# Kernel optimization log

Measured on AMD Instinct MI355X. Metric: run time of the kernel, lower is better.

## Reference

```python
import jax, jax.numpy as jnp
import numpy as np

N_NODES = 50000
N_EDGES = 800000
IN_DIM = 128
HIDDEN = 128
OUT_DIM = 40


def setup_inputs() -> dict:
    key = jax.random.key(0)
    ks = jax.random.split(key, 6)
    x = jax.random.normal(ks[0], (N_NODES, IN_DIM), dtype=jnp.float32)
    edge_src = jax.random.randint(ks[1], (N_EDGES,), 0, N_NODES, dtype=jnp.int32)
    edge_dst = jax.random.randint(ks[2], (N_EDGES,), 0, N_NODES, dtype=jnp.int32)
    edge_weight = jax.random.uniform(ks[3], (N_EDGES,), dtype=jnp.float32)
    W1 = jax.random.normal(ks[4], (IN_DIM, HIDDEN), dtype=jnp.float32) / np.sqrt(IN_DIM)
    b1 = jnp.zeros((HIDDEN,), dtype=jnp.float32)
    W2 = jax.random.normal(ks[5], (HIDDEN, OUT_DIM), dtype=jnp.float32) / np.sqrt(HIDDEN)
    b2 = jnp.zeros((OUT_DIM,), dtype=jnp.float32)
    return {"x": x, "edge_src": edge_src, "edge_dst": edge_dst,
            "edge_weight": edge_weight, "W1": W1, "b1": b1, "W2": W2, "b2": b2}


def _spmm(edge_src, edge_dst, edge_weight, x):
    # out[i] = sum_{e: dst==i} w_e * x[src_e]   (sparse adj @ x)
    msgs = edge_weight[:, None] * x[edge_src]  # [E, D] gather
    return jax.ops.segment_sum(msgs, edge_dst, num_segments=N_NODES)


def reference(x, edge_src, edge_dst, edge_weight, W1, b1, W2, b2):
    # dropout p=0.0 (eval): identity
    h = _spmm(edge_src, edge_dst, edge_weight, x)       # adj @ x
    h = jax.nn.relu(h @ W1 + b1)                        # lin1 + relu
    h = _spmm(edge_src, edge_dst, edge_weight, h)       # adj @ h
    return h @ W2 + b2                                  # lin2
```

## Files before the change

### kernel.cpp

```cpp
#include <hip/hip_runtime.h>
#include <hip/hip_bf16.h>

#define N_NODES 50000
#define N_EDGES 800000
#define IN_DIM 128
#define HIDDEN 128
#define OUT_DIM 40
#define G_STRIDE 64

#define SCAN_BS 1024
#define SCAN_BLOCKS ((N_NODES + SCAN_BS - 1) / SCAN_BS)

#define CHUNK_SHIFT 13
#define CHUNK 8192
#define NCHUNK 98
#define CNT_STRIDE 50176
#define CNT_WORDS (CNT_STRIDE / 4)

#define G1_ROWS 128
#define G1_BLOCKS ((N_NODES + G1_ROWS - 1) / G1_ROWS)
#define HG_GRID (NCHUNK + G1_BLOCKS)

struct __align__(8) Edge { int s; float w; };

typedef __attribute__((ext_vector_type(8))) short bf16x8;
typedef __attribute__((ext_vector_type(4))) float f32x4;
typedef __attribute__((ext_vector_type(8))) unsigned short u16x8;
typedef __attribute__((ext_vector_type(4))) unsigned short u16x4;

__device__ __forceinline__ unsigned f32_to_bf16_bits(float f) {
    unsigned u = __float_as_uint(f);
    return (u + 0x7FFFu + ((u >> 16) & 1u)) >> 16;
}
__device__ __forceinline__ float b2f(unsigned short u) {
    return __uint_as_float(((unsigned)u) << 16);
}

__global__ __launch_bounds__(512) void hist_gemm1(const int* __restrict__ dst,
                                                  unsigned char* __restrict__ cnt,
                                                  unsigned char* __restrict__ erank,
                                                  const float* __restrict__ x,
                                                  const float* __restrict__ W1,
                                                  __hip_bfloat16* __restrict__ y)
{
    __shared__ __align__(16) unsigned int shmem[CNT_WORDS];
    int bid = blockIdx.x;
    int t = threadIdx.x;

    if (bid < NCHUNK) {
        for (int f = t; f < CNT_WORDS; f += 512) shmem[f] = 0u;
        __syncthreads();
        int base = bid << CHUNK_SHIFT;
        #pragma unroll
        for (int r = 0; r < CHUNK / 512; ++r) {
            int i = base + r * 512 + t;
            if (i < N_EDGES) {
                int d = dst[i];
                unsigned sh = (unsigned)(d & 3) * 8u;
                unsigned old = atomicAdd(&shmem[d >> 2], 1u << sh);
                erank[i] = (unsigned char)((old >> sh) & 0xffu);
            }
        }
        __syncthreads();
        unsigned int* cw = (unsigned int*)(cnt + (size_t)bid * CNT_STRIDE);
        for (int f = t; f < CNT_WORDS; f += 512) cw[f] = shmem[f];
        return;
    }

    bf16x8* w1s = (bf16x8*)shmem;
    int gb = bid - NCHUNK;
    for (int f = t; f < 2048; f += 512) {
        int lane = f & 63;
        int nt = (f >> 6) & 7;
        int ks = f >> 9;
        int m = lane & 15, quad = lane >> 4;
        bf16x8 frag;
        #pragma unroll
        for (int j = 0; j < 8; ++j) {
            int k = ks * 32 + quad * 8 + j;
            frag[j] = (short)f32_to_bf16_bits(W1[k * HIDDEN + nt * 16 + m]);
        }
        w1s[f] = frag;
    }
    __syncthreads();

    int wv = t >> 6;
    int lane = t & 63;
    int m = lane & 15, quad = lane >> 4;
    int row0 = gb * G1_ROWS + wv * 16;
    int arow = row0 + m;
    if (arow >= N_NODES) arow = N_NODES - 1;

    bf16x8 afrag[4];
    #pragma unroll
    for (int ks = 0; ks < 4; ++ks) {
        const float4* xp = (const float4*)(x + (long long)arow * IN_DIM + ks * 32 + quad * 8);
        float4 a0 = xp[0], a1 = xp[1];
        afrag[ks][0] = (short)f32_to_bf16_bits(a0.x);
        afrag[ks][1] = (short)f32_to_bf16_bits(a0.y);
        afrag[ks][2] = (short)f32_to_bf16_bits(a0.z);
        afrag[ks][3] = (short)f32_to_bf16_bits(a0.w);
        afrag[ks][4] = (short)f32_to_bf16_bits(a1.x);
        afrag[ks][5] = (short)f32_to_bf16_bits(a1.y);
        afrag[ks][6] = (short)f32_to_bf16_bits(a1.z);
        afrag[ks][7] = (short)f32_to_bf16_bits(a1.w);
    }

    f32x4 acc[8];
    #pragma unroll
    for (int nt = 0; nt < 8; ++nt) acc[nt] = (f32x4){0.f, 0.f, 0.f, 0.f};

    #pragma unroll
    for (int ks = 0; ks < 4; ++ks) {
        #pragma unroll
        for (int nt = 0; nt < 8; ++nt) {
            bf16x8 bfrag = w1s[(ks * 8 + nt) * 64 + lane];
            acc[nt] = __builtin_amdgcn_mfma_f32_16x16x32_bf16(afrag[ks], bfrag, acc[nt], 0, 0, 0);
        }
    }

    #pragma unroll
    for (int nt = 0; nt < 8; ++nt) {
        #pragma unroll
        for (int r = 0; r < 4; ++r) {
            int rrow = row0 + quad * 4 + r;
            if (rrow < N_NODES)
                y[(long long)rrow * HIDDEN + nt * 16 + m] = __float2bfloat16(acc[nt][r]);
        }
    }
}

__global__ __launch_bounds__(SCAN_BS) void scan_fused(unsigned char* __restrict__ cnt,
                                                      int* __restrict__ row_ptr,
                                                      int* __restrict__ flags)
{
    __shared__ int tmp[SCAN_BS];
    __shared__ int red[SCAN_BS / 64];
    __shared__ int blk_off;
    int t = threadIdx.x;
    int bid = blockIdx.x;
    int i = bid * SCAN_BS + t;

    int total = 0;
    if (i < N_NODES) {
        int off = 0;
        for (int c = 0; c < NCHUNK; ++c) {
            unsigned char h = cnt[(size_t)c * CNT_STRIDE + i];
            cnt[(size_t)c * CNT_STRIDE + i] = (unsigned char)off;
            off += h;
        }
        total = off;
    }
    int s = total;
    for (int off = 32; off > 0; off >>= 1) s += __shfl_down(s, off, 64);
    int wave = t >> 6, lane = t & 63;
    if (lane == 0) red[wave] = s;
    __syncthreads();
    if (t == 0) {
        int tt = 0;
        #pragma unroll
        for (int wv = 0; wv < SCAN_BS / 64; ++wv) tt += red[wv];
        __hip_atomic_store(&flags[bid], tt + 1,
                           __ATOMIC_RELEASE, __HIP_MEMORY_SCOPE_AGENT);
    }
    if (t < 64) {
        int v2 = 0;
        if (t < bid) {
            int v;
            do {
                v = __hip_atomic_load(&flags[t],
                                      __ATOMIC_ACQUIRE, __HIP_MEMORY_SCOPE_AGENT);
            } while (v == 0);
            v2 = v - 1;
        }
        for (int off = 32; off > 0; off >>= 1) v2 += __shfl_down(v2, off, 64);
        if (t == 0) {
            blk_off = v2;
            if (bid == 0) row_ptr[N_NODES] = N_EDGES;
        }
    }
    int v = total;
    tmp[t] = v;
    __syncthreads();
    for (int off = 1; off < SCAN_BS; off <<= 1) {
        int u = (t >= off) ? tmp[t - off] : 0;
        __syncthreads();
        tmp[t] += u;
        __syncthreads();
    }
    if (i < N_NODES) row_ptr[i] = tmp[t] - v + blk_off;
}

__global__ __launch_bounds__(256) void scatter_det(const int* __restrict__ src,
                                                   const int* __restrict__ dst,
                                                   const float* __restrict__ w,
                                                   const unsigned char* __restrict__ cnt,
                                                   const unsigned char* __restrict__ erank,
                                                   const int* __restrict__ row_ptr,
                                                   Edge* __restrict__ edges)
{
    int i = blockIdx.x * 256 + threadIdx.x;
    int d = dst[i];
    int chunk = i >> CHUNK_SHIFT;
    int pos = row_ptr[d] + (int)cnt[(size_t)chunk * CNT_STRIDE + d] + (int)erank[i];
    Edge ed; ed.s = src[i]; ed.w = w[i];
    edges[pos] = ed;
}

__global__ __launch_bounds__(256) void spmm1_kernel(const int* __restrict__ row_ptr,
                                                    const Edge* __restrict__ edges,
                                                    const __hip_bfloat16* __restrict__ y,
                                                    const float* __restrict__ b1,
                                                    __hip_bfloat16* __restrict__ h1)
{
    int wv = threadIdx.x >> 6;
    int lane = threadIdx.x & 63;
    int grp = lane >> 4;
    int sub = lane & 15;
    int node = blockIdx.x * 16 + wv * 4 + grp;
    int j = row_ptr[node];
    int e = row_ptr[node + 1];

    float acc[8];
    #pragma unroll
    for (int k = 0; k < 8; ++k) acc[k] = 0.f;

    for (; j + 7 < e; j += 8) {
        Edge ed[8];
        #pragma unroll
        for (int u = 0; u < 8; ++u) ed[u] = edges[j + u];
        u16x8 v[8];
        #pragma unroll
        for (int u = 0; u < 8; ++u)
            v[u] = *(const u16x8*)(y + ((long long)ed[u].s << 7) + (sub << 3));
        #pragma unroll
        for (int u = 0; u < 8; ++u) {
            #pragma unroll
            for (int k = 0; k < 8; ++k)
                acc[k] = fmaf(ed[u].w, b2f(v[u][k]), acc[k]);
        }
    }
    for (; j + 3 < e; j += 4) {
        Edge ed[4];
        #pragma unroll
        for (int u = 0; u < 4; ++u) ed[u] = edges[j + u];
        u16x8 v[4];
        #pragma unroll
        for (int u = 0; u < 4; ++u)
            v[u] = *(const u16x8*)(y + ((long long)ed[u].s << 7) + (sub << 3));
        #pragma unroll
        for (int u = 0; u < 4; ++u) {
            #pragma unroll
            for (int k = 0; k < 8; ++k)
                acc[k] = fmaf(ed[u].w, b2f(v[u][k]), acc[k]);
        }
    }
    for (; j < e; ++j) {
        Edge ed0 = edges[j];
        u16x8 v0 = *(const u16x8*)(y + ((long long)ed0.s << 7) + (sub << 3));
        #pragma unroll
        for (int k = 0; k < 8; ++k)
            acc[k] = fmaf(ed0.w, b2f(v0[k]), acc[k]);
    }

    float4 bA = *(const float4*)(b1 + (sub << 3));
    float4 bB = *(const float4*)(b1 + (sub << 3) + 4);
    u16x8 hv;
    hv[0] = (unsigned short)f32_to_bf16_bits(fmaxf(acc[0] + bA.x, 0.f));
    hv[1] = (unsigned short)f32_to_bf16_bits(fmaxf(acc[1] + bA.y, 0.f));
    hv[2] = (unsigned short)f32_to_bf16_bits(fmaxf(acc[2] + bA.z, 0.f));
    hv[3] = (unsigned short)f32_to_bf16_bits(fmaxf(acc[3] + bA.w, 0.f));
    hv[4] = (unsigned short)f32_to_bf16_bits(fmaxf(acc[4] + bB.x, 0.f));
    hv[5] = (unsigned short)f32_to_bf16_bits(fmaxf(acc[5] + bB.y, 0.f));
    hv[6] = (unsigned short)f32_to_bf16_bits(fmaxf(acc[6] + bB.z, 0.f));
    hv[7] = (unsigned short)f32_to_bf16_bits(fmaxf(acc[7] + bB.w, 0.f));
    *(u16x8*)(h1 + ((long long)node << 7) + (sub << 3)) = hv;
}

__global__ __launch_bounds__(256) void gemm2_mfma(const __hip_bfloat16* __restrict__ h1,
                                                  const float* __restrict__ W2,
                                                  __hip_bfloat16* __restrict__ g)
{
    __shared__ bf16x8 w2s[768];
    int t = threadIdx.x;
    for (int f = t; f < 768; f += 256) {
        int lane = f & 63;
        int nt = (f >> 6) % 3;
        int ks = f / 192;
        int m = lane & 15, quad = lane >> 4;
        int col = nt * 16 + m;
        bf16x8 frag;
        #pragma unroll
        for (int j = 0; j < 8; ++j) {
            int k = ks * 32 + quad * 8 + j;
            float val = (col < OUT_DIM) ? W2[k * OUT_DIM + col] : 0.f;
            frag[j] = (short)f32_to_bf16_bits(val);
        }
        w2s[f] = frag;
    }
    __syncthreads();

    int wv = t >> 6;
    int lane = t & 63;
    int m = lane & 15, quad = lane >> 4;
    int row0 = blockIdx.x * 64 + wv * 16;
    int arow = row0 + m;
    if (arow >= N_NODES) arow = N_NODES - 1;

    bf16x8 afrag[4];
    #pragma unroll
    for (int ks = 0; ks < 4; ++ks)
        afrag[ks] = *(const bf16x8*)(h1 + (long long)arow * HIDDEN + ks * 32 + quad * 8);

    f32x4 acc[3];
    #pragma unroll
    for (int nt = 0; nt < 3; ++nt) acc[nt] = (f32x4){0.f, 0.f, 0.f, 0.f};

    #pragma unroll
    for (int ks = 0; ks < 4; ++ks) {
        #pragma unroll
        for (int nt = 0; nt < 3; ++nt) {
            bf16x8 bfrag = w2s[(ks * 3 + nt) * 64 + lane];
            acc[nt] = __builtin_amdgcn_mfma_f32_16x16x32_bf16(afrag[ks], bfrag, acc[nt], 0, 0, 0);
        }
    }

    #pragma unroll
    for (int nt = 0; nt < 3; ++nt) {
        int col = nt * 16 + m;
        if (col < OUT_DIM) {
            #pragma unroll
            for (int r = 0; r < 4; ++r) {
                int rrow = row0 + quad * 4 + r;
                if (rrow < N_NODES)
                    g[(rrow << 6) + col] = __float2bfloat16(acc[nt][r]);
            }
        }
    }
    if (m < 6) {
        u16x4 z = (u16x4){0, 0, 0, 0};
        #pragma unroll
        for (int r = 0; r < 4; ++r) {
            int rrow = row0 + quad * 4 + r;
            if (rrow < N_NODES)
                *(u16x4*)(g + (rrow << 6) + OUT_DIM + m * 4) = z;
        }
    }
}

__global__ __launch_bounds__(256) void spmm2_kernel(const int* __restrict__ row_ptr,
                                                    const Edge* __restrict__ edges,
                                                    const __hip_bfloat16* __restrict__ g,
                                                    const float* __restrict__ b2,
                                                    float* __restrict__ out)
{
    int wv = threadIdx.x >> 6;
    int lane = threadIdx.x & 63;
    int grp = lane >> 4;
    int sub = lane & 15;
    int node = blockIdx.x * 16 + wv * 4 + grp;
    int j = row_ptr[node];
    int e = row_ptr[node + 1];

    float acc[4];
    #pragma unroll
    for (int k = 0; k < 4; ++k) acc[k] = 0.f;

    for (; j + 7 < e; j += 8) {
        Edge ed[8];
        #pragma unroll
        for (int u = 0; u < 8; ++u) ed[u] = edges[j + u];
        u16x4 v[8];
        #pragma unroll
        for (int u = 0; u < 8; ++u)
            v[u] = *(const u16x4*)(g + ((long long)ed[u].s << 6) + (sub << 2));
        #pragma unroll
        for (int u = 0; u < 8; ++u) {
            #pragma unroll
            for (int k = 0; k < 4; ++k)
                acc[k] = fmaf(ed[u].w, b2f(v[u][k]), acc[k]);
        }
    }
    for (; j + 3 < e; j += 4) {
        Edge ed[4];
        #pragma unroll
        for (int u = 0; u < 4; ++u) ed[u] = edges[j + u];
        u16x4 v[4];
        #pragma unroll
        for (int u = 0; u < 4; ++u)
            v[u] = *(const u16x4*)(g + ((long long)ed[u].s << 6) + (sub << 2));
        #pragma unroll
        for (int u = 0; u < 4; ++u) {
            #pragma unroll
            for (int k = 0; k < 4; ++k)
                acc[k] = fmaf(ed[u].w, b2f(v[u][k]), acc[k]);
        }
    }
    for (; j < e; ++j) {
        Edge ed0 = edges[j];
        u16x4 v0 = *(const u16x4*)(g + ((long long)ed0.s << 6) + (sub << 2));
        #pragma unroll
        for (int k = 0; k < 4; ++k)
            acc[k] = fmaf(ed0.w, b2f(v0[k]), acc[k]);
    }

    if (sub < 10) {
        float4 bb = *(const float4*)(b2 + (sub << 2));
        float4 o;
        o.x = acc[0] + bb.x;
        o.y = acc[1] + bb.y;
        o.z = acc[2] + bb.z;
        o.w = acc[3] + bb.w;
        *(float4*)(out + (long long)node * OUT_DIM + (sub << 2)) = o;
    }
}

extern "C" void kernel_launch(void* const* d_in, const int* in_sizes, int n_in,
                              void* d_out, int out_size, void* d_ws, size_t ws_size,
                              hipStream_t stream)
{
    const float* x    = (const float*)d_in[0];
    const int*   esrc = (const int*)  d_in[1];
    const int*   edst = (const int*)  d_in[2];
    const float* ew   = (const float*)d_in[3];
    const float* W1   = (const float*)d_in[4];
    const float* b1   = (const float*)d_in[5];
    const float* W2   = (const float*)d_in[6];
    const float* b2   = (const float*)d_in[7];
    float* out = (float*)d_out;

    __hip_bfloat16* y  = (__hip_bfloat16*)d_ws;
    __hip_bfloat16* g  = y;
    __hip_bfloat16* h1 = y + (size_t)N_NODES * HIDDEN;
    Edge* edges     = (Edge*)(h1 + (size_t)N_NODES * HIDDEN);
    unsigned char* cnt   = (unsigned char*)(edges + N_EDGES);
    unsigned char* erank = cnt + (size_t)NCHUNK * CNT_STRIDE;
    int* row_ptr    = (int*)(erank + N_EDGES);
    int* flags      = row_ptr + 50176;

    hipMemsetAsync(flags, 0, 64 * sizeof(int), stream);
    hist_gemm1<<<HG_GRID, 512, 0, stream>>>(edst, cnt, erank, x, W1, y);
    scan_fused<<<SCAN_BLOCKS, SCAN_BS, 0, stream>>>(cnt, row_ptr, flags);
    scatter_det<<<N_EDGES / 256, 256, 0, stream>>>(esrc, edst, ew, cnt,
                                                   erank, row_ptr, edges);

    spmm1_kernel<<<N_NODES / 16, 256, 0, stream>>>(row_ptr, edges, y, b1, h1);
    gemm2_mfma<<<(N_NODES + 63) / 64, 256, 0, stream>>>(h1, W2, g);
    spmm2_kernel<<<N_NODES / 16, 256, 0, stream>>>(row_ptr, edges, g, b2, out);
}
```

Baseline: 181.3 us.

## Merge six kernels into two persistent launches with flag-based inter-stage waits

Combines histogram, gemm1, scan and scatter into one launch and spmm1, gemm2, spmm2 into a second launch. Later stages spin on global atomic counters until the earlier block ranges signal completion. This removes kernel launch gaps and lets independent work such as gemm1 overlap with histogram and scan. It relies on earlier-indexed blocks being scheduled before the waiting blocks, which risks deadlock or idle spinning blocks that hold CU slots.

```diff
diff --git a/kernel.cpp b/kernel.cpp
--- a/kernel.cpp
+++ b/kernel.cpp
@@ -8,18 +8,27 @@
 #define OUT_DIM 40
 #define G_STRIDE 64
 
-#define SCAN_BS 1024
-#define SCAN_BLOCKS ((N_NODES + SCAN_BS - 1) / SCAN_BS)
-
 #define CHUNK_SHIFT 13
 #define CHUNK 8192
 #define NCHUNK 98
 #define CNT_STRIDE 50176
 #define CNT_WORDS (CNT_STRIDE / 4)
 
-#define G1_ROWS 128
-#define G1_BLOCKS ((N_NODES + G1_ROWS - 1) / G1_ROWS)
-#define HG_GRID (NCHUNK + G1_BLOCKS)
+#define HB 98
+#define GB 391
+#define SB 98
+#define CB 1563
+#define D1_GRID (HB + GB + SB + CB)
+#define M_SPMM1 3125
+#define M_GEMM2 782
+#define M_SPMM2 3125
+#define D2_GRID (M_SPMM1 + M_GEMM2 + M_SPMM2)
+
+#define FD_HIST 0
+#define FD_SCAN 1
+#define FD_SPMM1 2
+#define FD_GEMM2 3
+#define FD_SCANBLK 8
 
 struct __align__(8) Edge { int s; float w; };
 
@@ -36,18 +45,32 @@
     return __uint_as_float(((unsigned)u) << 16);
 }
 
-__global__ __launch_bounds__(512) void hist_gemm1(const int* __restrict__ dst,
-                                                  unsigned char* __restrict__ cnt,
-                                                  unsigned char* __restrict__ erank,
-                                                  const float* __restrict__ x,
-                                                  const float* __restrict__ W1,
-                                                  __hip_bfloat16* __restrict__ y)
+__device__ __forceinline__ void wait_ge(int* p, int target) {
+    while (__hip_atomic_load(p, __ATOMIC_RELAXED, __HIP_MEMORY_SCOPE_AGENT) < target)
+        __builtin_amdgcn_s_sleep(32);
+    (void)__hip_atomic_load(p, __ATOMIC_ACQUIRE, __HIP_MEMORY_SCOPE_AGENT);
+}
+__device__ __forceinline__ void signal_done(int* p) {
+    __hip_atomic_fetch_add(p, 1, __ATOMIC_RELEASE, __HIP_MEMORY_SCOPE_AGENT);
+}
+
+__global__ __launch_bounds__(512) void csr_gemm1(const int* __restrict__ dst,
+                                                 const int* __restrict__ src,
+                                                 const float* __restrict__ w,
+                                                 unsigned char* __restrict__ cnt,
+                                                 unsigned char* __restrict__ erank,
+                                                 const float* __restrict__ x,
+                                                 const float* __restrict__ W1,
+                                                 __hip_bfloat16* __restrict__ y,
+                                                 int* __restrict__ row_ptr,
+                                                 Edge* __restrict__ edges,
+                                                 int* __restrict__ flags)
 {
     __shared__ __align__(16) unsigned int shmem[CNT_WORDS];
     int bid = blockIdx.x;
     int t = threadIdx.x;
 
-    if (bid < NCHUNK) {
+    if (bid < HB) {
         for (int f = t; f < CNT_WORDS; f += 512) shmem[f] = 0u;
         __syncthreads();
         int base = bid << CHUNK_SHIFT;
@@ -64,354 +87,374 @@
         __syncthreads();
         unsigned int* cw = (unsigned int*)(cnt + (size_t)bid * CNT_STRIDE);
         for (int f = t; f < CNT_WORDS; f += 512) cw[f] = shmem[f];
+        __syncthreads();
+        if (t == 0) signal_done(&flags[FD_HIST]);
         return;
     }
 
-    bf16x8* w1s = (bf16x8*)shmem;
-    int gb = bid - NCHUNK;
-    for (int f = t; f < 2048; f += 512) {
-        int lane = f & 63;
-        int nt = (f >> 6) & 7;
-        int ks = f >> 9;
+    if (bid < HB + GB) {
+        bf16x8* w1s = (bf16x8*)shmem;
+        int gb = bid - HB;
+        for (int f = t; f < 2048; f += 512) {
+            int lane = f & 63;
+            int nt = (f >> 6) & 7;
+            int ks = f >> 9;
+            int m = lane & 15, quad = lane >> 4;
+            bf16x8 frag;
+            #pragma unroll
+            for (int j = 0; j < 8; ++j) {
+                int k = ks * 32 + quad * 8 + j;
+                frag[j] = (short)f32_to_bf16_bits(W1[k * HIDDEN + nt * 16 + m]);
+            }
+            w1s[f] = frag;
+        }
+        __syncthreads();
+
+        int wv = t >> 6;
+        int lane = t & 63;
         int m = lane & 15, quad = lane >> 4;
-        bf16x8 frag;
-        #pragma unroll
-        for (int j = 0; j < 8; ++j) {
-            int k = ks * 32 + quad * 8 + j;
-            frag[j] = (short)f32_to_bf16_bits(W1[k * HIDDEN + nt * 16 + m]);
-        }
-        w1s[f] = frag;
-    }
-    __syncthreads();
-
-    int wv = t >> 6;
-    int lane = t & 63;
-    int m = lane & 15, quad = lane >> 4;
-    int row0 = gb * G1_ROWS + wv * 16;
-    int arow = row0 + m;
-    if (arow >= N_NODES) arow = N_NODES - 1;
-
-    bf16x8 afrag[4];
-    #pragma unroll
-    for (int ks = 0; ks < 4; ++ks) {
-        const float4* xp = (const float4*)(x + (long long)arow * IN_DIM + ks * 32 + quad * 8);
-        float4 a0 = xp[0], a1 = xp[1];
-        afrag[ks][0] = (short)f32_to_bf16_bits(a0.x);
-        afrag[ks][1] = (short)f32_to_bf16_bits(a0.y);
-        afrag[ks][2] = (short)f32_to_bf16_bits(a0.z);
-        afrag[ks][3] = (short)f32_to_bf16_bits(a0.w);
-        afrag[ks][4] = (short)f32_to_bf16_bits(a1.x);
-        afrag[ks][5] = (short)f32_to_bf16_bits(a1.y);
-        afrag[ks][6] = (short)f32_to_bf16_bits(a1.z);
-        afrag[ks][7] = (short)f32_to_bf16_bits(a1.w);
-    }
-
-    f32x4 acc[8];
-    #pragma unroll
-    for (int nt = 0; nt < 8; ++nt) acc[nt] = (f32x4){0.f, 0.f, 0.f, 0.f};
-
-    #pragma unroll
-    for (int ks = 0; ks < 4; ++ks) {
+        int row0 = gb * 128 + wv * 16;
+        int arow = row0 + m;
+        if (arow >= N_NODES) arow = N_NODES - 1;
+
+        bf16x8 afrag[4];
+        #pragma unroll
+        for (int ks = 0; ks < 4; ++ks) {
+            const float4* xp = (const float4*)(x + (long long)arow * IN_DIM + ks * 32 + quad * 8);
+            float4 a0 = xp[0], a1 = xp[1];
+            afrag[ks][0] = (short)f32_to_bf16_bits(a0.x);
+            afrag[ks][1] = (short)f32_to_bf16_bits(a0.y);
+            afrag[ks][2] = (short)f32_to_bf16_bits(a0.z);
+            afrag[ks][3] = (short)f32_to_bf16_bits(a0.w);
+            afrag[ks][4] = (short)f32_to_bf16_bits(a1.x);
+            afrag[ks][5] = (short)f32_to_bf16_bits(a1.y);
+            afrag[ks][6] = (short)f32_to_bf16_bits(a1.z);
+            afrag[ks][7] = (short)f32_to_bf16_bits(a1.w);
+        }
+
+        f32x4 acc[8];
+        #pragma unroll
+        for (int nt = 0; nt < 8; ++nt) acc[nt] = (f32x4){0.f, 0.f, 0.f, 0.f};
+
+        #pragma unroll
+        for (int ks = 0; ks < 4; ++ks) {
+            #pragma unroll
+            for (int nt = 0; nt < 8; ++nt) {
+                bf16x8 bfrag = w1s[(ks * 8 + nt) * 64 + lane];
+                acc[nt] = __builtin_amdgcn_mfma_f32_16x16x32_bf16(afrag[ks], bfrag, acc[nt], 0, 0, 0);
+            }
+        }
+
         #pragma unroll
         for (int nt = 0; nt < 8; ++nt) {
-            bf16x8 bfrag = w1s[(ks * 8 + nt) * 64 + lane];
-            acc[nt] = __builtin_amdgcn_mfma_f32_16x16x32_bf16(afrag[ks], bfrag, acc[nt], 0, 0, 0);
-        }
-    }
-
-    #pragma unroll
-    for (int nt = 0; nt < 8; ++nt) {
-        #pragma unroll
-        for (int r = 0; r < 4; ++r) {
-            int rrow = row0 + quad * 4 + r;
-            if (rrow < N_NODES)
-                y[(long long)rrow * HIDDEN + nt * 16 + m] = __float2bfloat16(acc[nt][r]);
-        }
-    }
-}
-
-__global__ __launch_bounds__(SCAN_BS) void scan_fused(unsigned char* __restrict__ cnt,
-                                                      int* __restrict__ row_ptr,
-                                                      int* __restrict__ flags)
-{
-    __shared__ int tmp[SCAN_BS];
-    __shared__ int red[SCAN_BS / 64];
-    __shared__ int blk_off;
-    int t = threadIdx.x;
-    int bid = blockIdx.x;
-    int i = bid * SCAN_BS + t;
-
-    int total = 0;
-    if (i < N_NODES) {
-        int off = 0;
-        for (int c = 0; c < NCHUNK; ++c) {
-            unsigned char h = cnt[(size_t)c * CNT_STRIDE + i];
-            cnt[(size_t)c * CNT_STRIDE + i] = (unsigned char)off;
-            off += h;
-        }
-        total = off;
-    }
-    int s = total;
-    for (int off = 32; off > 0; off >>= 1) s += __shfl_down(s, off, 64);
-    int wave = t >> 6, lane = t & 63;
-    if (lane == 0) red[wave] = s;
-    __syncthreads();
-    if (t == 0) {
-        int tt = 0;
-        #pragma unroll
-        for (int wv = 0; wv < SCAN_BS / 64; ++wv) tt += red[wv];
-        __hip_atomic_store(&flags[bid], tt + 1,
-                           __ATOMIC_RELEASE, __HIP_MEMORY_SCOPE_AGENT);
-    }
-    if (t < 64) {
-        int v2 = 0;
-        if (t < bid) {
-            int v;
-            do {
-                v = __hip_atomic_load(&flags[t],
-                                      __ATOMIC_ACQUIRE, __HIP_MEMORY_SCOPE_AGENT);
-            } while (v == 0);
-            v2 = v - 1;
-        }
-        for (int off = 32; off > 0; off >>= 1) v2 += __shfl_down(v2, off, 64);
-        if (t == 0) {
-            blk_off = v2;
-            if (bid == 0) row_ptr[N_NODES] = N_EDGES;
-        }
-    }
-    int v = total;
-    tmp[t] = v;
-    __syncthreads();
-    for (int off = 1; off < SCAN_BS; off <<= 1) {
-        int u = (t >= off) ? tmp[t - off] : 0;
-        __syncthreads();
-        tmp[t] += u;
-        __syncthreads();
-    }
-    if (i < N_NODES) row_ptr[i] = tmp[t] - v + blk_off;
-}
-
-__global__ __launch_bounds__(256) void scatter_det(const int* __restrict__ src,
-                                                   const int* __restrict__ dst,
-                                                   const float* __restrict__ w,
-                                                   const unsigned char* __restrict__ cnt,
-                                                   const unsigned char* __restrict__ erank,
-                                                   const int* __restrict__ row_ptr,
-                                                   Edge* __restrict__ edges)
-{
-    int i = blockIdx.x * 256 + threadIdx.x;
-    int d = dst[i];
-    int chunk = i >> CHUNK_SHIFT;
-    int pos = row_ptr[d] + (int)cnt[(size_t)chunk * CNT_STRIDE + d] + (int)erank[i];
-    Edge ed; ed.s = src[i]; ed.w = w[i];
-    edges[pos] = ed;
-}
-
-__global__ __launch_bounds__(256) void spmm1_kernel(const int* __restrict__ row_ptr,
-                                                    const Edge* __restrict__ edges,
-                                                    const __hip_bfloat16* __restrict__ y,
-                                                    const float* __restrict__ b1,
-                                                    __hip_bfloat16* __restrict__ h1)
-{
-    int wv = threadIdx.x >> 6;
-    int lane = threadIdx.x & 63;
-    int grp = lane >> 4;
-    int sub = lane & 15;
-    int node = blockIdx.x * 16 + wv * 4 + grp;
-    int j = row_ptr[node];
-    int e = row_ptr[node + 1];
-
-    float acc[8];
-    #pragma unroll
-    for (int k = 0; k < 8; ++k) acc[k] = 0.f;
-
-    for (; j + 7 < e; j += 8) {
-        Edge ed[8];
-        #pragma unroll
-        for (int u = 0; u < 8; ++u) ed[u] = edges[j + u];
-        u16x8 v[8];
-        #pragma unroll
-        for (int u = 0; u < 8; ++u)
-            v[u] = *(const u16x8*)(y + ((long long)ed[u].s << 7) + (sub << 3));
-        #pragma unroll
-        for (int u = 0; u < 8; ++u) {
-            #pragma unroll
-            for (int k = 0; k < 8; ++k)
-                acc[k] = fmaf(ed[u].w, b2f(v[u][k]), acc[k]);
-        }
-    }
-    for (; j + 3 < e; j += 4) {
-        Edge ed[4];
-        #pragma unroll
-        for (int u = 0; u < 4; ++u) ed[u] = edges[j + u];
-        u16x8 v[4];
-        #pragma unroll
-        for (int u = 0; u < 4; ++u)
-            v[u] = *(const u16x8*)(y + ((long long)ed[u].s << 7) + (sub << 3));
-        #pragma unroll
-        for (int u = 0; u < 4; ++u) {
-            #pragma unroll
-            for (int k = 0; k < 8; ++k)
-                acc[k] = fmaf(ed[u].w, b2f(v[u][k]), acc[k]);
-        }
-    }
-    for (; j < e; ++j) {
-        Edge ed0 = edges[j];
-        u16x8 v0 = *(const u16x8*)(y + ((long long)ed0.s << 7) + (sub << 3));
-        #pragma unroll
-        for (int k = 0; k < 8; ++k)
-            acc[k] = fmaf(ed0.w, b2f(v0[k]), acc[k]);
-    }
-
-    float4 bA = *(const float4*)(b1 + (sub << 3));
-    float4 bB = *(const float4*)(b1 + (sub << 3) + 4);
-    u16x8 hv;
-    hv[0] = (unsigned short)f32_to_bf16_bits(fmaxf(acc[0] + bA.x, 0.f));
-    hv[1] = (unsigned short)f32_to_bf16_bits(fmaxf(acc[1] + bA.y, 0.f));
-    hv[2] = (unsigned short)f32_to_bf16_bits(fmaxf(acc[2] + bA.z, 0.f));
-    hv[3] = (unsigned short)f32_to_bf16_bits(fmaxf(acc[3] + bA.w, 0.f));
-    hv[4] = (unsigned short)f32_to_bf16_bits(fmaxf(acc[4] + bB.x, 0.f));
-    hv[5] = (unsigned short)f32_to_bf16_bits(fmaxf(acc[5] + bB.y, 0.f));
-    hv[6] = (unsigned short)f32_to_bf16_bits(fmaxf(acc[6] + bB.z, 0.f));
-    hv[7] = (unsigned short)f32_to_bf16_bits(fmaxf(acc[7] + bB.w, 0.f));
-    *(u16x8*)(h1 + ((long long)node << 7) + (sub << 3)) = hv;
-}
-
-__global__ __launch_bounds__(256) void gemm2_mfma(const __hip_bfloat16* __restrict__ h1,
-                                                  const float* __restrict__ W2,
-                                                  __hip_bfloat16* __restrict__ g)
-{
-    __shared__ bf16x8 w2s[768];
-    int t = threadIdx.x;
-    for (int f = t; f < 768; f += 256) {
-        int lane = f & 63;
-        int nt = (f >> 6) % 3;
-        int ks = f / 192;
-        int m = lane & 15, quad = lane >> 4;
-        int col = nt * 16 + m;
-        bf16x8 frag;
-        #pragma unroll
-        for (int j = 0; j < 8; ++j) {
-            int k = ks * 32 + quad * 8 + j;
-            float val = (col < OUT_DIM) ? W2[k * OUT_DIM + col] : 0.f;
-            frag[j] = (short)f32_to_bf16_bits(val);
-        }
-        w2s[f] = frag;
-    }
-    __syncthreads();
-
-    int wv = t >> 6;
-    int lane = t & 63;
-    int m = lane & 15, quad = lane >> 4;
-    int row0 = blockIdx.x * 64 + wv * 16;
-    int arow = row0 + m;
-    if (arow >= N_NODES) arow = N_NODES - 1;
-
-    bf16x8 afrag[4];
-    #pragma unroll
-    for (int ks = 0; ks < 4; ++ks)
-        afrag[ks] = *(const bf16x8*)(h1 + (long long)arow * HIDDEN + ks * 32 + quad * 8);
-
-    f32x4 acc[3];
-    #pragma unroll
-    for (int nt = 0; nt < 3; ++nt) acc[nt] = (f32x4){0.f, 0.f, 0.f, 0.f};
-
-    #pragma unroll
-    for (int ks = 0; ks < 4; ++ks) {
-        #pragma unroll
-        for (int nt = 0; nt < 3; ++nt) {
-            bf16x8 bfrag = w2s[(ks * 3 + nt) * 64 + lane];
-            acc[nt] = __builtin_amdgcn_mfma_f32_16x16x32_bf16(afrag[ks], bfrag, acc[nt], 0, 0, 0);
-        }
-    }
-
-    #pragma unroll
-    for (int nt = 0; nt < 3; ++nt) {
-        int col = nt * 16 + m;
-        if (col < OUT_DIM) {
             #pragma unroll
             for (int r = 0; r < 4; ++r) {
                 int rrow = row0 + quad * 4 + r;
                 if (rrow < N_NODES)
-                    g[(rrow << 6) + col] = __float2bfloat16(acc[nt][r]);
-            }
-        }
-    }
-    if (m < 6) {
-        u16x4 z = (u16x4){0, 0, 0, 0};
-        #pragma unroll
-        for (int r = 0; r < 4; ++r) {
-            int rrow = row0 + quad * 4 + r;
-            if (rrow < N_NODES)
-                *(u16x4*)(g + (rrow << 6) + OUT_DIM + m * 4) = z;
-        }
-    }
-}
-
-__global__ __launch_bounds__(256) void spmm2_kernel(const int* __restrict__ row_ptr,
-                                                    const Edge* __restrict__ edges,
-                                                    const __hip_bfloat16* __restrict__ g,
-                                                    const float* __restrict__ b2,
-                                                    float* __restrict__ out)
+                    y[(long long)rrow * HIDDEN + nt * 16 + m] = __float2bfloat16(acc[nt][r]);
+            }
+        }
+        return;
+    }
+
+    if (bid < HB + GB + SB) {
+        int sb = bid - HB - GB;
+        int* tmp  = (int*)shmem;
+        int* red  = tmp + 512;
+        int* red2 = red + 8;
+        if (t == 0) wait_ge(&flags[FD_HIST], HB);
+        __syncthreads();
+
+        int i = sb * 512 + t;
+        int total = 0;
+        if (i < N_NODES) {
+            int off = 0;
+            for (int c = 0; c < NCHUNK; ++c) {
+                unsigned char h = cnt[(size_t)c * CNT_STRIDE + i];
+                cnt[(size_t)c * CNT_STRIDE + i] = (unsigned char)off;
+                off += h;
+            }
+            total = off;
+        }
+        int s = total;
+        for (int off = 32; off > 0; off >>= 1) s += __shfl_down(s, off, 64);
+        int wave = t >> 6, lane = t & 63;
+        if (lane == 0) red[wave] = s;
+        __syncthreads();
+        if (t == 0) {
+            int tt = 0;
+            #pragma unroll
+            for (int wv = 0; wv < 8; ++wv) tt += red[wv];
+            __hip_atomic_store(&flags[FD_SCANBLK + sb], tt + 1,
+                               __ATOMIC_RELEASE, __HIP_MEMORY_SCOPE_AGENT);
+        }
+        if (t < 128) {
+            int v2 = 0;
+            if (t < sb) {
+                int v;
+                do {
+                    v = __hip_atomic_load(&flags[FD_SCANBLK + t],
+                                          __ATOMIC_ACQUIRE, __HIP_MEMORY_SCOPE_AGENT);
+                } while (v == 0);
+                v2 = v - 1;
+            }
+            for (int off = 32; off > 0; off >>= 1) v2 += __shfl_down(v2, off, 64);
+            if ((t & 63) == 0) red2[t >> 6] = v2;
+        }
+        __syncthreads();
+        int blk_off = red2[0] + red2[1];
+        __syncthreads();
+        int v = total;
+        tmp[t] = v;
+        __syncthreads();
+        for (int off = 1; off < 512; off <<= 1) {
+            int u = (t >= off) ? tmp[t - off] : 0;
+            __syncthreads();
+            tmp[t] += u;
+            __syncthreads();
+        }
+        if (i < N_NODES) row_ptr[i] = tmp[t] - v + blk_off;
+        if (sb == 0 && t == 0) row_ptr[N_NODES] = N_EDGES;
+        __syncthreads();
+        if (t == 0) signal_done(&flags[FD_SCAN]);
+        return;
+    }
+
+    {
+        int cb = bid - HB - GB - SB;
+        if (t == 0) wait_ge(&flags[FD_SCAN], SB);
+        __syncthreads();
+        int i = cb * 512 + t;
+        if (i < N_EDGES) {
+            int d = dst[i];
+            int chunk = i >> CHUNK_SHIFT;
+            int pos = row_ptr[d] + (int)cnt[(size_t)chunk * CNT_STRIDE + d] + (int)erank[i];
+            Edge ed; ed.s = src[i]; ed.w = w[i];
+            edges[pos] = ed;
+        }
+    }
+}
+
+__global__ __launch_bounds__(256) void mlp_spmm(const int* __restrict__ row_ptr,
+                                                const Edge* __restrict__ edges,
+                                                const __hip_bfloat16* __restrict__ y,
+                                                const float* __restrict__ b1,
+                                                __hip_bfloat16* __restrict__ h1,
+                                                const float* __restrict__ W2,
+                                                __hip_bfloat16* __restrict__ g,
+                                                const float* __restrict__ b2,
+                                                float* __restrict__ out,
+                                                int* __restrict__ flags)
 {
-    int wv = threadIdx.x >> 6;
-    int lane = threadIdx.x & 63;
-    int grp = lane >> 4;
-    int sub = lane & 15;
-    int node = blockIdx.x * 16 + wv * 4 + grp;
-    int j = row_ptr[node];
-    int e = row_ptr[node + 1];
-
-    float acc[4];
-    #pragma unroll
-    for (int k = 0; k < 4; ++k) acc[k] = 0.f;
-
-    for (; j + 7 < e; j += 8) {
-        Edge ed[8];
-        #pragma unroll
-        for (int u = 0; u < 8; ++u) ed[u] = edges[j + u];
-        u16x4 v[8];
-        #pragma unroll
-        for (int u = 0; u < 8; ++u)
-            v[u] = *(const u16x4*)(g + ((long long)ed[u].s << 6) + (sub << 2));
-        #pragma unroll
-        for (int u = 0; u < 8; ++u) {
+    __shared__ bf16x8 w2s[768];
+    int bid = blockIdx.x;
+    int t = threadIdx.x;
+
+    if (bid < M_SPMM1) {
+        int wv = t >> 6;
+        int lane = t & 63;
+        int grp = lane >> 4;
+        int sub = lane & 15;
+        int node = bid * 16 + wv * 4 + grp;
+        int j = row_ptr[node];
+        int e = row_ptr[node + 1];
+
+        float acc[8];
+        #pragma unroll
+        for (int k = 0; k < 8; ++k) acc[k] = 0.f;
+
+        for (; j + 7 < e; j += 8) {
+            Edge ed[8];
+            #pragma unroll
+            for (int u = 0; u < 8; ++u) ed[u] = edges[j + u];
+            u16x8 v[8];
+            #pragma unroll
+            for (int u = 0; u < 8; ++u)
+                v[u] = *(const u16x8*)(y + ((long long)ed[u].s << 7) + (sub << 3));
+            #pragma unroll
+            for (int u = 0; u < 8; ++u) {
+                #pragma unroll
+                for (int k = 0; k < 8; ++k)
+                    acc[k] = fmaf(ed[u].w, b2f(v[u][k]), acc[k]);
+            }
+        }
+        for (; j + 3 < e; j += 4) {
+            Edge ed[4];
+            #pragma unroll
+            for (int u = 0; u < 4; ++u) ed[u] = edges[j + u];
+            u16x8 v[4];
+            #pragma unroll
+            for (int u = 0; u < 4; ++u)
+                v[u] = *(const u16x8*)(y + ((long long)ed[u].s << 7) + (sub << 3));
+            #pragma unroll
+            for (int u = 0; u < 4; ++u) {
+                #pragma unroll
+                for (int k = 0; k < 8; ++k)
+                    acc[k] = fmaf(ed[u].w, b2f(v[u][k]), acc[k]);
+            }
+        }
+        for (; j < e; ++j) {
+            Edge ed0 = edges[j];
+            u16x8 v0 = *(const u16x8*)(y + ((long long)ed0.s << 7) + (sub << 3));
+            #pragma unroll
+            for (int k = 0; k < 8; ++k)
+                acc[k] = fmaf(ed0.w, b2f(v0[k]), acc[k]);
+        }
+
+        float4 bA = *(const float4*)(b1 + (sub << 3));
+        float4 bB = *(const float4*)(b1 + (sub << 3) + 4);
+        u16x8 hv;
+        hv[0] = (unsigned short)f32_to_bf16_bits(fmaxf(acc[0] + bA.x, 0.f));
+        hv[1] = (unsigned short)f32_to_bf16_bits(fmaxf(acc[1] + bA.y, 0.f));
+        hv[2] = (unsigned short)f32_to_bf16_bits(fmaxf(acc[2] + bA.z, 0.f));
+        hv[3] = (unsigned short)f32_to_bf16_bits(fmaxf(acc[3] + bA.w, 0.f));
+        hv[4] = (unsigned short)f32_to_bf16_bits(fmaxf(acc[4] + bB.x, 0.f));
+        hv[5] = (unsigned short)f32_to_bf16_bits(fmaxf(acc[5] + bB.y, 0.f));
+        hv[6] = (unsigned short)f32_to_bf16_bits(fmaxf(acc[6] + bB.z, 0.f));
+        hv[7] = (unsigned short)f32_to_bf16_bits(fmaxf(acc[7] + bB.w, 0.f));
+        *(u16x8*)(h1 + ((long long)node << 7) + (sub << 3)) = hv;
+        __syncthreads();
+        if (t == 0) signal_done(&flags[FD_SPMM1]);
+        return;
+    }
+
+    if (bid < M_SPMM1 + M_GEMM2) {
+        int gb = bid - M_SPMM1;
+        if (t == 0) wait_ge(&flags[FD_SPMM1], M_SPMM1);
+        __syncthreads();
+
+        for (int f = t; f < 768; f += 256) {
+            int lane = f & 63;
+            int nt = (f >> 6) % 3;
+            int ks = f / 192;
+            int m = lane & 15, quad = lane >> 4;
+            int col = nt * 16 + m;
+            bf16x8 frag;
+            #pragma unroll
+            for (int j = 0; j < 8; ++j) {
+                int k = ks * 32 + quad * 8 + j;
+                float val = (col < OUT_DIM) ? W2[k * OUT_DIM + col] : 0.f;
+                frag[j] = (short)f32_to_bf16_bits(val);
+            }
+            w2s[f] = frag;
+        }
+        __syncthreads();
+
+        int wv = t >> 6;
+        int lane = t & 63;
+        int m = lane & 15, quad = lane >> 4;
+        int row0 = gb * 64 + wv * 16;
+        int arow = row0 + m;
+        if (arow >= N_NODES) arow = N_NODES - 1;
+
+        bf16x8 afrag[4];
+        #pragma unroll
+        for (int ks = 0; ks < 4; ++ks)
+            afrag[ks] = *(const bf16x8*)(h1 + (long long)arow * HIDDEN + ks * 32 + quad * 8);
+
+        f32x4 acc[3];
+        #pragma unroll
+        for (int nt = 0; nt < 3; ++nt) acc[nt] = (f32x4){0.f, 0.f, 0.f, 0.f};
+
+        #pragma unroll
+        for (int ks = 0; ks < 4; ++ks) {
+            #pragma unroll
+            for (int nt = 0; nt < 3; ++nt) {
+                bf16x8 bfrag = w2s[(ks * 3 + nt) * 64 + lane];
+                acc[nt] = __builtin_amdgcn_mfma_f32_16x16x32_bf16(afrag[ks], bfrag, acc[nt], 0, 0, 0);
+            }
+        }
+
+        #pragma unroll
+        for (int nt = 0; nt < 3; ++nt) {
+            int col = nt * 16 + m;
+            if (col < OUT_DIM) {
+                #pragma unroll
+                for (int r = 0; r < 4; ++r) {
+                    int rrow = row0 + quad * 4 + r;
+                    if (rrow < N_NODES)
+                        g[(rrow << 6) + col] = __float2bfloat16(acc[nt][r]);
+                }
+            }
+        }
+        if (m < 6) {
+            u16x4 z = (u16x4){0, 0, 0, 0};
+            #pragma unroll
+            for (int r = 0; r < 4; ++r) {
+                int rrow = row0 + quad * 4 + r;
+                if (rrow < N_NODES)
+                    *(u16x4*)(g + (rrow << 6) + OUT_DIM + m * 4) = z;
+            }
+        }
+        __syncthreads();
+        if (t == 0) signal_done(&flags[FD_GEMM2]);
+        return;
+    }
+
+    {
+        int sb2 = bid - M_SPMM1 - M_GEMM2;
+        if (t == 0) wait_ge(&flags[FD_GEMM2], M_GEMM2);
+        __syncthreads();
+
+        int wv = t >> 6;
+        int lane = t & 63;
+        int grp = lane >> 4;
+        int sub = lane & 15;
+        int node = sb2 * 16 + wv * 4 + grp;
+        int j = row_ptr[node];
+        int e = row_ptr[node + 1];
+
+        float acc[4];
+        #pragma unroll
+        for (int k = 0; k < 4; ++k) acc[k] = 0.f;
+
+        for (; j + 7 < e; j += 8) {
+            Edge ed[8];
+            #pragma unroll
+            for (int u = 0; u < 8; ++u) ed[u] = edges[j + u];
+            u16x4 v[8];
+            #pragma unroll
+            for (int u = 0; u < 8; ++u)
+                v[u] = *(const u16x4*)(g + ((long long)ed[u].s << 6) + (sub << 2));
+            #pragma unroll
+            for (int u = 0; u < 8; ++u) {
+                #pragma unroll
+                for (int k = 0; k < 4; ++k)
+                    acc[k] = fmaf(ed[u].w, b2f(v[u][k]), acc[k]);
+            }
+        }
+        for (; j + 3 < e; j += 4) {
+            Edge ed[4];
+            #pragma unroll
+            for (int u = 0; u < 4; ++u) ed[u] = edges[j + u];
+            u16x4 v[4];
+            #pragma unroll
+            for (int u = 0; u < 4; ++u)
+                v[u] = *(const u16x4*)(g + ((long long)ed[u].s << 6) + (sub << 2));
+            #pragma unroll
+            for (int u = 0; u < 4; ++u) {
+                #pragma unroll
+                for (int k = 0; k < 4; ++k)
+                    acc[k] = fmaf(ed[u].w, b2f(v[u][k]), acc[k]);
+            }
+        }
+        for (; j < e; ++j) {
+            Edge ed0 = edges[j];
+            u16x4 v0 = *(const u16x4*)(g + ((long long)ed0.s << 6) + (sub << 2));
             #pragma unroll
             for (int k = 0; k < 4; ++k)
-                acc[k] = fmaf(ed[u].w, b2f(v[u][k]), acc[k]);
-        }
-    }
-    for (; j + 3 < e; j += 4) {
-        Edge ed[4];
-        #pragma unroll
-        for (int u = 0; u < 4; ++u) ed[u] = edges[j + u];
-        u16x4 v[4];
-        #pragma unroll
-        for (int u = 0; u < 4; ++u)
-            v[u] = *(const u16x4*)(g + ((long long)ed[u].s << 6) + (sub << 2));
-        #pragma unroll
-        for (int u = 0; u < 4; ++u) {
-            #pragma unroll
-            for (int k = 0; k < 4; ++k)
-                acc[k] = fmaf(ed[u].w, b2f(v[u][k]), acc[k]);
-        }
-    }
-    for (; j < e; ++j) {
-        Edge ed0 = edges[j];
-        u16x4 v0 = *(const u16x4*)(g + ((long long)ed0.s << 6) + (sub << 2));
-        #pragma unroll
-        for (int k = 0; k < 4; ++k)
-            acc[k] = fmaf(ed0.w, b2f(v0[k]), acc[k]);
-    }
-
-    if (sub < 10) {
-        float4 bb = *(const float4*)(b2 + (sub << 2));
-        float4 o;
-        o.x = acc[0] + bb.x;
-        o.y = acc[1] + bb.y;
-        o.z = acc[2] + bb.z;
-        o.w = acc[3] + bb.w;
-        *(float4*)(out + (long long)node * OUT_DIM + (sub << 2)) = o;
+                acc[k] = fmaf(ed0.w, b2f(v0[k]), acc[k]);
+        }
+
+        if (sub < 10) {
+            float4 bb = *(const float4*)(b2 + (sub << 2));
+            float4 o;
+            o.x = acc[0] + bb.x;
+            o.y = acc[1] + bb.y;
+            o.z = acc[2] + bb.z;
+            o.w = acc[3] + bb.w;
+            *(float4*)(out + (long long)node * OUT_DIM + (sub << 2)) = o;
+        }
     }
 }
 
@@ -438,13 +481,9 @@
     int* row_ptr    = (int*)(erank + N_EDGES);
     int* flags      = row_ptr + 50176;
 
-    hipMemsetAsync(flags, 0, 64 * sizeof(int), stream);
-    hist_gemm1<<<HG_GRID, 512, 0, stream>>>(edst, cnt, erank, x, W1, y);
-    scan_fused<<<SCAN_BLOCKS, SCAN_BS, 0, stream>>>(cnt, row_ptr, flags);
-    scatter_det<<<N_EDGES / 256, 256, 0, stream>>>(esrc, edst, ew, cnt,
-                                                   erank, row_ptr, edges);
-
-    spmm1_kernel<<<N_NODES / 16, 256, 0, stream>>>(row_ptr, edges, y, b1, h1);
-    gemm2_mfma<<<(N_NODES + 63) / 64, 256, 0, stream>>>(h1, W2, g);
-    spmm2_kernel<<<N_NODES / 16, 256, 0, stream>>>(row_ptr, edges, g, b2, out);
-}
+    hipMemsetAsync(flags, 0, 128 * sizeof(int), stream);
+    csr_gemm1<<<D1_GRID, 512, 0, stream>>>(edst, esrc, ew, cnt, erank,
+                                           x, W1, y, row_ptr, edges, flags);
+    mlp_spmm<<<D2_GRID, 256, 0, stream>>>(row_ptr, edges, y, b1, h1,
+                                          W2, g, b2, out, flags);
+}
```

New measurement: 433.7 us. +139.2%, slower.
